# Optimization experiments

Measured on AMD Instinct MI355X. Metric: run time of the kernel, lower is better.

Reference implementation:

```python
import jax, jax.numpy as jnp
import numpy as np

N_RAYS = 65536
N_SAMPLES = 2_097_152
HID = 64
L_PTS, L_DIR = 10, 4
STEP = 5e-3
WHITE_BKGD = True


def posenc(x, L):
    # x [..., 3] -> [..., 3 + 6L]
    freqs = (2.0 ** jnp.arange(L)).astype(x.dtype)            # [L]
    ang = x[..., None, :] * freqs[:, None]                     # [..., L, 3]
    enc = jnp.concatenate([jnp.sin(ang), jnp.cos(ang)], -1)   # [..., L, 6]
    return jnp.concatenate([x, enc.reshape(x.shape[:-1] + (6 * L,))], -1)


def setup_inputs() -> dict:
    key = jax.random.key(0)
    ks = jax.random.split(key, 12)
    rays_o = jax.random.normal(ks[0], (N_RAYS, 3), jnp.float32)
    viewdirs = jax.random.normal(ks[1], (N_RAYS, 3), jnp.float32)
    viewdirs = viewdirs / jnp.linalg.norm(viewdirs, axis=-1, keepdims=True)
    ray_indices = jnp.sort(jax.random.randint(ks[2], (N_SAMPLES,), 0, N_RAYS, jnp.int32))
    t_starts = jax.random.uniform(ks[3], (N_SAMPLES,), jnp.float32, 0.0, 4.0)
    t_ends = t_starts + STEP

    def w(k, shape):
        return jax.random.normal(k, shape, jnp.float32) / jnp.sqrt(shape[0])

    D_PTS = 3 + 6 * L_PTS   # 63
    D_DIR = 3 + 6 * L_DIR   # 27
    return dict(
        rays_o=rays_o, viewdirs=viewdirs, t_starts=t_starts, t_ends=t_ends,
        W1=w(ks[4], (D_PTS, HID)), b1=jnp.zeros((HID,), jnp.float32),
        W2=w(ks[5], (HID, HID)), b2=jnp.zeros((HID,), jnp.float32),
        Wd=w(ks[6], (HID, 1)), bd=jnp.zeros((1,), jnp.float32),
        Wf=w(ks[7], (HID, HID)), bf=jnp.zeros((HID,), jnp.float32),
        Wr1=w(ks[8], (HID + D_DIR, HID)), br1=jnp.zeros((HID,), jnp.float32),
        Wr2=w(ks[9], (HID, 3)), br2=jnp.zeros((3,), jnp.float32),
        ray_indices=ray_indices,
    )


def reference(rays_o, viewdirs, t_starts, t_ends,
              W1, b1, W2, b2, Wd, bd, Wf, bf, Wr1, br1, Wr2, br2,
              ray_indices):
    t_mid = 0.5 * (t_starts + t_ends)                     # [S]
    o = rays_o[ray_indices]                               # gather [S,3]
    d = viewdirs[ray_indices]                             # gather [S,3]
    pts = o + d * t_mid[:, None]                          # [S,3]

    # small NeRF MLP (self.net): sigma + view-dependent rgb
    h = jax.nn.relu(posenc(pts, L_PTS) @ W1 + b1)
    h = jax.nn.relu(h @ W2 + b2)
    sigma = jax.nn.relu((h @ Wd + bd)[:, 0])              # relu(density)
    feat = h @ Wf + bf
    hd = jax.nn.relu(jnp.concatenate([feat, posenc(d, L_DIR)], -1) @ Wr1 + br1)
    rgb = jax.nn.sigmoid(hd @ Wr2 + br2)                  # [S,3]

    alpha = 1.0 - jnp.exp(-sigma * (t_ends - t_starts))   # [S], in [0,1)

    # per-ray exclusive transmittance via segment exclusive cumsum in log space
    log1m = jnp.log1p(-jnp.clip(alpha, 0.0, 1.0 - 1e-7))  # <= 0
    excl = jnp.cumsum(log1m) - log1m                      # global exclusive cumsum
    counts = jax.ops.segment_sum(jnp.ones_like(ray_indices), ray_indices, N_RAYS)
    start_idx = jnp.cumsum(counts) - counts               # first sample of each ray
    offset = jnp.where(counts > 0, excl[jnp.clip(start_idx, 0, N_SAMPLES - 1)], 0.0)
    T = jnp.exp(excl - offset[ray_indices])               # transmittance [S]
    w = T * alpha                                         # render weights [S]

    colors = jax.ops.segment_sum(w[:, None] * rgb, ray_indices, N_RAYS)   # [R,3]
    opac = jax.ops.segment_sum(w, ray_indices, N_RAYS)                    # [R]
    depth = jax.ops.segment_sum(w * t_mid, ray_indices, N_RAYS)           # [R]

    bkgd = 1.0 if WHITE_BKGD else 0.0
    colors = colors + (1.0 - opac)[:, None] * bkgd
    return colors, opac[:, None], depth[:, None]
```

## Files before the change

### kernel.cpp

```cpp
#include <hip/hip_runtime.h>
#include <math.h>

#define NR 65536
#define NS 2097152

typedef __attribute__((ext_vector_type(4))) float f32x4;
typedef __attribute__((ext_vector_type(2))) float f32x2;
typedef __attribute__((ext_vector_type(8))) short short8;

#define RSTRIDE 36
#define GSTRIDE (16 * 36 + 4)


__device__ __forceinline__ uint packbf(float a, float b) {
    __bf16 lo = (__bf16)a, hi = (__bf16)b;
    ushort ul = __builtin_bit_cast(ushort, lo);
    ushort uh = __builtin_bit_cast(ushort, hi);
    return (uint)ul | ((uint)uh << 16);
}
__device__ __forceinline__ float bflo(uint u) { return __builtin_bit_cast(float, u << 16); }

__global__ void setup_kernel(const float* __restrict__ viewdirs,
                             uint4* __restrict__ dtab,
                             int* __restrict__ start, int* __restrict__ end,
                             const float* __restrict__ W1, const float* __restrict__ W2,
                             const float* __restrict__ Wf, const float* __restrict__ Wr1,
                             const float* __restrict__ Wd, const float* __restrict__ Wr2,
                             uint4* __restrict__ wfrag) {
    int b = blockIdx.x, tid = threadIdx.x;
    if (b < 256) {
        int r = b * 256 + tid;
        float dx = viewdirs[3 * r + 0], dy = viewdirs[3 * r + 1], dz = viewdirs[3 * r + 2];
        float de[32];
        de[0] = dx; de[1] = dy; de[2] = dz;
        float sx = __sinf(dx), cx = __cosf(dx);
        float sy = __sinf(dy), cy = __cosf(dy);
        float sz = __sinf(dz), cz = __cosf(dz);
        #pragma unroll
        for (int l = 0; l < 4; ++l) {
            de[3 + 6 * l + 0] = sx; de[3 + 6 * l + 1] = sy; de[3 + 6 * l + 2] = sz;
            de[3 + 6 * l + 3] = cx; de[3 + 6 * l + 4] = cy; de[3 + 6 * l + 5] = cz;
            float nsx = 2.0f * sx * cx, nsy = 2.0f * sy * cy, nsz = 2.0f * sz * cz;
            cx = fmaf(-2.0f * sx, sx, 1.0f);
            cy = fmaf(-2.0f * sy, sy, 1.0f);
            cz = fmaf(-2.0f * sz, sz, 1.0f);
            sx = nsx; sy = nsy; sz = nsz;
        }
        #pragma unroll
        for (int k = 27; k < 32; ++k) de[k] = 0.0f;
        #pragma unroll
        for (int c = 0; c < 4; ++c) {
            uint4 q = make_uint4(packbf(de[8 * c + 0], de[8 * c + 1]),
                                 packbf(de[8 * c + 2], de[8 * c + 3]),
                                 packbf(de[8 * c + 4], de[8 * c + 5]),
                                 packbf(de[8 * c + 6], de[8 * c + 7]));
            dtab[(size_t)r * 4 + c] = q;
        }
    } else if (b < 512) {
        int r = (b - 256) * 256 + tid;
        start[r] = 0; end[r] = 0;
    } else {
        int t = (b - 512) * 256 + tid;
        if (t >= 40 * 64) return;
        int f = t >> 6, lane = t & 63;
        int c = lane & 15;
        uint q[4];
        if (f < 36) {
            const float* W; int kmax, fl;
            if (f < 8)       { W = W1;  kmax = 63; fl = f; }
            else if (f < 16) { W = W2;  kmax = 64; fl = f - 8; }
            else if (f < 24) { W = Wf;  kmax = 64; fl = f - 16; }
            else             { W = Wr1; kmax = 91; fl = f - 24; }
            int ks = fl >> 2, ft = fl & 3;
            int n = ft * 16 + c;
            int kb = ks * 32 + ((lane >> 4) * 8);
            #pragma unroll
            for (int j = 0; j < 4; ++j) {
                int k0 = kb + 2 * j, k1 = k0 + 1;
                float v0 = (k0 < kmax) ? W[k0 * 64 + n] : 0.0f;
                float v1 = (k1 < kmax) ? W[k1 * 64 + n] : 0.0f;
                q[j] = packbf(v0, v1);
            }
        } else if (f < 38) {
            int kb = (f - 36) * 32 + ((lane >> 4) * 8);
            #pragma unroll
            for (int j = 0; j < 4; ++j) {
                float v0 = (c == 0) ? Wd[kb + 2 * j] : 0.0f;
                float v1 = (c == 0) ? Wd[kb + 2 * j + 1] : 0.0f;
                q[j] = packbf(v0, v1);
            }
        } else {
            int kb = (f - 38) * 32 + ((lane >> 4) * 8);
            #pragma unroll
            for (int j = 0; j < 4; ++j) {
                float v0 = (c < 3) ? Wr2[(kb + 2 * j) * 3 + c] : 0.0f;
                float v1 = (c < 3) ? Wr2[(kb + 2 * j + 1) * 3 + c] : 0.0f;
                q[j] = packbf(v0, v1);
            }
        }
        wfrag[(size_t)f * 64 + lane] = make_uint4(q[0], q[1], q[2], q[3]);
    }
}


template <int KS, bool RELU, bool SIGMA, bool DIRB>
__device__ __forceinline__ void dense_layer(uint* S, const uint4* __restrict__ wfrag,
                                            int fb, const float* __restrict__ bias,
                                            float bd0, uint rbase, uint wbA, uint wbB,
                                            int lane, const uint4 (&dirB)[4]) {
    const int g = lane >> 4;
    uint4 wf[KS * 4];
    #pragma unroll
    for (int i = 0; i < KS * 4; ++i) wf[i] = wfrag[(size_t)(fb + i) * 64 + lane];
    uint4 wsg[2];
    if constexpr (SIGMA) {
        wsg[0] = wfrag[36 * 64 + lane];
        wsg[1] = wfrag[37 * 64 + lane];
    }
    float4 bfr[4];
    #pragma unroll
    for (int ft = 0; ft < 4; ++ft)
        bfr[ft] = *(const float4*)(bias + 16 * ft + 4 * g);

    #pragma unroll
    for (int st = 0; st < 4; ++st) {
        const uint stoff = (uint)st * (uint)GSTRIDE;
        uint4 B[KS];
        #pragma unroll
        for (int ks = 0; ks < KS; ++ks) {
            if (DIRB && ks == KS - 1) B[ks] = dirB[st];
            else B[ks] = *(const uint4*)&S[rbase + stoff + 16u * (uint)ks];
        }
        f32x4 acc[4];
        #pragma unroll
        for (int ft = 0; ft < 4; ++ft)
            acc[ft] = (f32x4){bfr[ft].x, bfr[ft].y, bfr[ft].z, bfr[ft].w};
        f32x4 sacc;
        if constexpr (SIGMA) sacc = (f32x4){(g == 0) ? bd0 : 0.0f, 0.0f, 0.0f, 0.0f};
        #pragma unroll
        for (int ks = 0; ks < KS; ++ks) {
            short8 bv = __builtin_bit_cast(short8, B[ks]);
            #pragma unroll
            for (int ft = 0; ft < 4; ++ft)
                acc[ft] = __builtin_amdgcn_mfma_f32_16x16x32_bf16(
                    __builtin_bit_cast(short8, wf[ks * 4 + ft]), bv, acc[ft], 0, 0, 0);
            if constexpr (SIGMA)
                sacc = __builtin_amdgcn_mfma_f32_16x16x32_bf16(
                    __builtin_bit_cast(short8, wsg[ks]), bv, sacc, 0, 0, 0);
        }
        #pragma unroll
        for (int ft = 0; ft < 4; ++ft) {
            f32x2 lo = {acc[ft][0], acc[ft][1]};
            f32x2 hi = {acc[ft][2], acc[ft][3]};
            if constexpr (RELU) {
                lo = __builtin_elementwise_max(lo, (f32x2){0.0f, 0.0f});
                hi = __builtin_elementwise_max(hi, (f32x2){0.0f, 0.0f});
            }
            uint2 v = make_uint2(packbf(lo.x, lo.y), packbf(hi.x, hi.y));
            uint base = (ft & 1) ? wbB : wbA;
            *(uint2*)&S[base + stoff + 16u * (uint)(ft >> 1)] = v;
        }
        if constexpr (SIGMA) {
            if (g == 0) S[rbase + stoff + 33u] = __builtin_bit_cast(uint, sacc[0]);
        }
    }
}

__global__ __launch_bounds__(256, 4) void fused_mlp(
    const float* __restrict__ rays_o, const float* __restrict__ viewdirs,
    const float* __restrict__ t_starts, const float* __restrict__ t_ends,
    const float* __restrict__ b1, const float* __restrict__ b2,
    const float* __restrict__ bd, const float* __restrict__ bf_,
    const float* __restrict__ br1, const float* __restrict__ br2,
    const int* __restrict__ ridx, const uint4* __restrict__ wfrag,
    const uint4* __restrict__ dtab, uint2* __restrict__ rgba,
    float* __restrict__ tmarr, int* __restrict__ start, int* __restrict__ end)
{
    __shared__ uint S[16 * GSTRIDE];

    const int tid = threadIdx.x;
    const int w = tid >> 6, lane = tid & 63;
    const int g = lane >> 4, s = lane & 15;
    const uint wgb = (uint)(w * 4) * (uint)GSTRIDE;
    const uint rowcol = wgb + (uint)s * (uint)RSTRIDE;
    const int sb0 = blockIdx.x * 256 + w * 64;

    int ridx4[4];
    #pragma unroll
    for (int st = 0; st < 4; ++st) ridx4[st] = ridx[sb0 + st * 16 + s];
    uint4 dirB[4];
    #pragma unroll
    for (int st = 0; st < 4; ++st) dirB[st] = dtab[(size_t)ridx4[st] * 4 + g];

    const int si = sb0 + g * 16 + s;
    const int rr = ridx4[g];

    {
        int r_prev = ridx[(si == 0) ? 0 : si - 1];
        int r_next = ridx[(si == NS - 1) ? NS - 1 : si + 1];
        if (si == 0 || r_prev != rr) start[rr] = si;
        if (si == NS - 1 || r_next != rr) end[rr] = si + 1;
    }

    float ts = t_starts[si], te = t_ends[si];
    float tm = 0.5f * (ts + te), dtv = te - ts;
    float dx = viewdirs[3 * rr + 0], dy = viewdirs[3 * rr + 1], dz = viewdirs[3 * rr + 2];
    float px = rays_o[3 * rr + 0] + dx * tm;
    float py = rays_o[3 * rr + 1] + dy * tm;
    float pz = rays_o[3 * rr + 2] + dz * tm;
    tmarr[si] = tm;

    const uint ownrow = wgb + (uint)g * (uint)GSTRIDE + (uint)s * (uint)RSTRIDE;
    const uint rbase = rowcol + 4u * (uint)g;
    const uint wbA = rowcol + 2u * (uint)g;
    const uint wbB = wbA + 8u;

    {
        float enc[64];
        enc[0] = px; enc[1] = py; enc[2] = pz;
        f32x2 sxy = {__sinf(px), __sinf(py)};
        f32x2 cxy = {__cosf(px), __cosf(py)};
        float sz = __sinf(pz), cz = __cosf(pz);
        #pragma unroll
        for (int l = 0; l < 10; ++l) {
            enc[3 + 6 * l + 0] = sxy.x; enc[3 + 6 * l + 1] = sxy.y; enc[3 + 6 * l + 2] = sz;
            enc[3 + 6 * l + 3] = cxy.x; enc[3 + 6 * l + 4] = cxy.y; enc[3 + 6 * l + 5] = cz;
            f32x2 nsxy = 2.0f * sxy * cxy;
            cxy = 1.0f - 2.0f * sxy * sxy;
            float nsz = 2.0f * sz * cz;
            cz = fmaf(-2.0f * sz, sz, 1.0f);
            sxy = nsxy; sz = nsz;
        }
        enc[63] = 0.0f;
        #pragma unroll
        for (int ch = 0; ch < 8; ++ch) {
            uint4 q = make_uint4(packbf(enc[8 * ch + 0], enc[8 * ch + 1]),
                                 packbf(enc[8 * ch + 2], enc[8 * ch + 3]),
                                 packbf(enc[8 * ch + 4], enc[8 * ch + 5]),
                                 packbf(enc[8 * ch + 6], enc[8 * ch + 7]));
            *(uint4*)&S[ownrow + 4u * (uint)ch] = q;
        }
    }
    S[ownrow + 32] = __builtin_bit_cast(uint, dtv);

    float bd0 = bd[0];
    uint4 dummy[4];

    dense_layer<2, true,  false, false>(S, wfrag,  0, b1,  0.0f, rbase, wbA, wbB, lane, dummy);
    dense_layer<2, true,  false, false>(S, wfrag,  8, b2,  0.0f, rbase, wbA, wbB, lane, dummy);
    dense_layer<2, false, true,  false>(S, wfrag, 16, bf_, bd0,  rbase, wbA, wbB, lane, dummy);
    dense_layer<3, true,  false, true >(S, wfrag, 24, br1, 0.0f, rbase, wbA, wbB, lane, dirB);

    {
        uint4 wr0 = wfrag[38 * 64 + lane], wr1f = wfrag[39 * 64 + lane];
        float c0 = br2[0], c1 = br2[1], c2 = br2[2];
        #pragma unroll
        for (int st = 0; st < 4; ++st) {
            const uint stoff = (uint)st * (uint)GSTRIDE;
            uint4 B0 = *(const uint4*)&S[rbase + stoff];
            uint4 B1 = *(const uint4*)&S[rbase + stoff + 16u];
            f32x4 acc = (g == 0) ? (f32x4){c0, c1, c2, 0.0f}
                                 : (f32x4){0.0f, 0.0f, 0.0f, 0.0f};
            acc = __builtin_amdgcn_mfma_f32_16x16x32_bf16(
                __builtin_bit_cast(short8, wr0), __builtin_bit_cast(short8, B0), acc, 0, 0, 0);
            acc = __builtin_amdgcn_mfma_f32_16x16x32_bf16(
                __builtin_bit_cast(short8, wr1f), __builtin_bit_cast(short8, B1), acc, 0, 0, 0);
            if (lane < 16) {
                uint2 meta = *(const uint2*)&S[rbase + stoff + 32u];
                float dte = __builtin_bit_cast(float, meta.x);
                float sg = fmaxf(__builtin_bit_cast(float, meta.y), 0.0f);
                float alpha = 1.0f - __expf(-sg * dte);
                float r0 = 1.0f / (1.0f + __expf(-acc[0]));
                float r1 = 1.0f / (1.0f + __expf(-acc[1]));
                float r2 = 1.0f / (1.0f + __expf(-acc[2]));
                uint2 o;
                o.x = packbf(r0, r1);
                o.y = packbf(r2, alpha);
                rgba[sb0 + st * 16 + lane] = o;
            }
        }
    }
}

__global__ void render_kernel(const uint2* __restrict__ rgba,
                              const float* __restrict__ tmarr,
                              const int* __restrict__ start,
                              const int* __restrict__ end,
                              float* __restrict__ out)
{
    int r = blockIdx.x * blockDim.x + threadIdx.x;
    if (r >= NR) return;
    int sb = start[r], e = end[r];
    float T = 1.0f, c0 = 0.0f, c1 = 0.0f, c2 = 0.0f, op = 0.0f, dp = 0.0f;
    for (int i = sb; i < e; ++i) {
        uint2 q = rgba[i];
        float tmid = tmarr[i];
        float vr = bflo(q.x & 0xffffu), vg = bflo(q.x >> 16);
        float vb = bflo(q.y & 0xffffu), va = bflo(q.y >> 16);
        float wgt = T * va;
        c0 += wgt * vr; c1 += wgt * vg; c2 += wgt * vb;
        op += wgt; dp += wgt * tmid;
        T *= (1.0f - va);
    }
    float bg = 1.0f - op;
    c0 += bg; c1 += bg; c2 += bg;
    out[3 * r + 0] = c0;
    out[3 * r + 1] = c1;
    out[3 * r + 2] = c2;
    out[3 * NR + r] = op;
    out[4 * NR + r] = dp;
}

extern "C" void kernel_launch(void* const* d_in, const int* in_sizes, int n_in,
                              void* d_out, int out_size, void* d_ws, size_t ws_size,
                              hipStream_t stream) {
    const float* rays_o   = (const float*)d_in[0];
    const float* viewdirs = (const float*)d_in[1];
    const float* t_starts = (const float*)d_in[2];
    const float* t_ends   = (const float*)d_in[3];
    const float* W1  = (const float*)d_in[4];
    const float* b1  = (const float*)d_in[5];
    const float* W2  = (const float*)d_in[6];
    const float* b2  = (const float*)d_in[7];
    const float* Wd  = (const float*)d_in[8];
    const float* bd  = (const float*)d_in[9];
    const float* Wf  = (const float*)d_in[10];
    const float* bf_ = (const float*)d_in[11];
    const float* Wr1 = (const float*)d_in[12];
    const float* br1 = (const float*)d_in[13];
    const float* Wr2 = (const float*)d_in[14];
    const float* br2 = (const float*)d_in[15];
    const int* ridx  = (const int*)d_in[16];
    float* out = (float*)d_out;

    char* ws = (char*)d_ws;
    uint2* rgba  = (uint2*)ws;
    float* tmarr = (float*)(ws + (size_t)NS * 8);
    int* start   = (int*)(ws + (size_t)NS * 12);
    int* end     = start + NR;
    uint4* wfrag = (uint4*)(ws + (size_t)NS * 12 + (size_t)NR * 8);
    uint4* dtab  = (uint4*)(ws + (size_t)NS * 12 + (size_t)NR * 8 + 40 * 64 * 16);

    setup_kernel<<<522, 256, 0, stream>>>(viewdirs, dtab, start, end,
                                          W1, W2, Wf, Wr1, Wd, Wr2, wfrag);
    fused_mlp<<<NS / 256, 256, 0, stream>>>(
        rays_o, viewdirs, t_starts, t_ends,
        b1, b2, bd, bf_, br1, br2, ridx, wfrag, dtab, rgba, tmarr, start, end);
    render_kernel<<<NR / 256, 256, 0, stream>>>(rgba, tmarr, start, end, out);
}
```

Baseline: 141.2 us.

## Use XOR-swizzled LDS layout, keep sigma/dt in registers, raise occupancy

Replaces the padded LDS row layout (stride 36 words) with a dense 32-word row layout that uses an XOR swizzle on 16-byte chunks to avoid bank conflicts. This shrinks shared memory per block from about 9.3K to 8K words. Sigma now stays in registers from the sigma layer and dt is fetched by a cross-lane shuffle, so neither makes a round trip through LDS. Launch bounds rise from 4 to 5 blocks per CU to exploit the smaller footprint, which risks register pressure or spills.

```diff
diff --git a/kernel.cpp b/kernel.cpp
--- a/kernel.cpp
+++ b/kernel.cpp
@@ -8,8 +8,6 @@
 typedef __attribute__((ext_vector_type(2))) float f32x2;
 typedef __attribute__((ext_vector_type(8))) short short8;
 
-#define RSTRIDE 36
-#define GSTRIDE (16 * 36 + 4)
 
 
 __device__ __forceinline__ uint packbf(float a, float b) {
@@ -102,12 +100,13 @@
     }
 }
 
-
 template <int KS, bool RELU, bool SIGMA, bool DIRB>
 __device__ __forceinline__ void dense_layer(uint* S, const uint4* __restrict__ wfrag,
                                             int fb, const float* __restrict__ bias,
-                                            float bd0, uint rbase, uint wbA, uint wbB,
-                                            int lane, const uint4 (&dirB)[4]) {
+                                            float bd0, const uint (&ro)[2],
+                                            const uint (&wo)[4],
+                                            int lane, const uint4 (&dirB)[4],
+                                            float* sigout) {
     const int g = lane >> 4;
     uint4 wf[KS * 4];
     #pragma unroll
@@ -124,12 +123,12 @@
 
     #pragma unroll
     for (int st = 0; st < 4; ++st) {
-        const uint stoff = (uint)st * (uint)GSTRIDE;
+        const uint stoff = (uint)st * 512u;
         uint4 B[KS];
         #pragma unroll
         for (int ks = 0; ks < KS; ++ks) {
             if (DIRB && ks == KS - 1) B[ks] = dirB[st];
-            else B[ks] = *(const uint4*)&S[rbase + stoff + 16u * (uint)ks];
+            else B[ks] = *(const uint4*)&S[ro[ks] + stoff];
         }
         f32x4 acc[4];
         #pragma unroll
@@ -157,16 +156,13 @@
                 hi = __builtin_elementwise_max(hi, (f32x2){0.0f, 0.0f});
             }
             uint2 v = make_uint2(packbf(lo.x, lo.y), packbf(hi.x, hi.y));
-            uint base = (ft & 1) ? wbB : wbA;
-            *(uint2*)&S[base + stoff + 16u * (uint)(ft >> 1)] = v;
-        }
-        if constexpr (SIGMA) {
-            if (g == 0) S[rbase + stoff + 33u] = __builtin_bit_cast(uint, sacc[0]);
-        }
-    }
-}
-
-__global__ __launch_bounds__(256, 4) void fused_mlp(
+            *(uint2*)&S[wo[ft] + stoff] = v;
+        }
+        if constexpr (SIGMA) sigout[st] = sacc[0];
+    }
+}
+
+__global__ __launch_bounds__(256, 5) void fused_mlp(
     const float* __restrict__ rays_o, const float* __restrict__ viewdirs,
     const float* __restrict__ t_starts, const float* __restrict__ t_ends,
     const float* __restrict__ b1, const float* __restrict__ b2,
@@ -176,13 +172,14 @@
     const uint4* __restrict__ dtab, uint2* __restrict__ rgba,
     float* __restrict__ tmarr, int* __restrict__ start, int* __restrict__ end)
 {
-    __shared__ uint S[16 * GSTRIDE];
+    __shared__ uint S[8192];
 
     const int tid = threadIdx.x;
     const int w = tid >> 6, lane = tid & 63;
     const int g = lane >> 4, s = lane & 15;
-    const uint wgb = (uint)(w * 4) * (uint)GSTRIDE;
-    const uint rowcol = wgb + (uint)s * (uint)RSTRIDE;
+    const uint sm = (uint)(s & 7);
+    const uint wgb = (uint)w * 2048u;
+    const uint rowb = wgb + (uint)s * 32u;
     const int sb0 = blockIdx.x * 256 + w * 64;
 
     int ridx4[4];
@@ -210,10 +207,14 @@
     float pz = rays_o[3 * rr + 2] + dz * tm;
     tmarr[si] = tm;
 
-    const uint ownrow = wgb + (uint)g * (uint)GSTRIDE + (uint)s * (uint)RSTRIDE;
-    const uint rbase = rowcol + 4u * (uint)g;
-    const uint wbA = rowcol + 2u * (uint)g;
-    const uint wbB = wbA + 8u;
+    const uint ownbase = wgb + (uint)g * 512u + (uint)s * 32u;
+    uint ro[2], wo[4];
+    #pragma unroll
+    for (int ks = 0; ks < 2; ++ks)
+        ro[ks] = rowb + 4u * (((uint)(g + 4 * ks)) ^ sm);
+    #pragma unroll
+    for (int ft = 0; ft < 4; ++ft)
+        wo[ft] = rowb + 4u * (((uint)(2 * ft + (g >> 1))) ^ sm) + 2u * (uint)(g & 1);
 
     {
         float enc[64];
@@ -238,37 +239,36 @@
                                  packbf(enc[8 * ch + 2], enc[8 * ch + 3]),
                                  packbf(enc[8 * ch + 4], enc[8 * ch + 5]),
                                  packbf(enc[8 * ch + 6], enc[8 * ch + 7]));
-            *(uint4*)&S[ownrow + 4u * (uint)ch] = q;
-        }
-    }
-    S[ownrow + 32] = __builtin_bit_cast(uint, dtv);
-
+            *(uint4*)&S[ownbase + 4u * (((uint)ch) ^ sm)] = q;
+        }
+    }
+
+    float sig4[4];
     float bd0 = bd[0];
     uint4 dummy[4];
 
-    dense_layer<2, true,  false, false>(S, wfrag,  0, b1,  0.0f, rbase, wbA, wbB, lane, dummy);
-    dense_layer<2, true,  false, false>(S, wfrag,  8, b2,  0.0f, rbase, wbA, wbB, lane, dummy);
-    dense_layer<2, false, true,  false>(S, wfrag, 16, bf_, bd0,  rbase, wbA, wbB, lane, dummy);
-    dense_layer<3, true,  false, true >(S, wfrag, 24, br1, 0.0f, rbase, wbA, wbB, lane, dirB);
+    dense_layer<2, true,  false, false>(S, wfrag,  0, b1,  0.0f, ro, wo, lane, dummy, sig4);
+    dense_layer<2, true,  false, false>(S, wfrag,  8, b2,  0.0f, ro, wo, lane, dummy, sig4);
+    dense_layer<2, false, true,  false>(S, wfrag, 16, bf_, bd0,  ro, wo, lane, dummy, sig4);
+    dense_layer<3, true,  false, true >(S, wfrag, 24, br1, 0.0f, ro, wo, lane, dirB, sig4);
 
     {
         uint4 wr0 = wfrag[38 * 64 + lane], wr1f = wfrag[39 * 64 + lane];
         float c0 = br2[0], c1 = br2[1], c2 = br2[2];
         #pragma unroll
         for (int st = 0; st < 4; ++st) {
-            const uint stoff = (uint)st * (uint)GSTRIDE;
-            uint4 B0 = *(const uint4*)&S[rbase + stoff];
-            uint4 B1 = *(const uint4*)&S[rbase + stoff + 16u];
+            const uint stoff = (uint)st * 512u;
+            uint4 B0 = *(const uint4*)&S[ro[0] + stoff];
+            uint4 B1 = *(const uint4*)&S[ro[1] + stoff];
             f32x4 acc = (g == 0) ? (f32x4){c0, c1, c2, 0.0f}
                                  : (f32x4){0.0f, 0.0f, 0.0f, 0.0f};
             acc = __builtin_amdgcn_mfma_f32_16x16x32_bf16(
                 __builtin_bit_cast(short8, wr0), __builtin_bit_cast(short8, B0), acc, 0, 0, 0);
             acc = __builtin_amdgcn_mfma_f32_16x16x32_bf16(
                 __builtin_bit_cast(short8, wr1f), __builtin_bit_cast(short8, B1), acc, 0, 0, 0);
+            float dte = __shfl(dtv, st * 16 + (lane & 15));
             if (lane < 16) {
-                uint2 meta = *(const uint2*)&S[rbase + stoff + 32u];
-                float dte = __builtin_bit_cast(float, meta.x);
-                float sg = fmaxf(__builtin_bit_cast(float, meta.y), 0.0f);
+                float sg = fmaxf(sig4[st], 0.0f);
                 float alpha = 1.0f - __expf(-sg * dte);
                 float r0 = 1.0f / (1.0f + __expf(-acc[0]));
                 float r1 = 1.0f / (1.0f + __expf(-acc[1]));
```

New measurement: 229.8 us. 1.63x slower.
